# Kernel optimization log

Measured on AMD Instinct MI355X. Metric: run time of the kernel, lower is better.

Reference implementation:

```python
import jax, jax.numpy as jnp
import numpy as np

# current_extent = radius * config.KP_extent / config.conv_radius = 0.1*1.2/2.5
KP_EXTENT = 0.1 * 1.2 / 2.5
BN_EPS = 1e-5  # InstanceNorm1d default eps (BatchNormBlock normalizes over points)
LEAKY_SLOPE = 0.1


def setup_inputs() -> dict:
    key = jax.random.key(0)
    ks = jax.random.split(key, 6)
    N, H, K, C_in, C_out = 100000, 32, 15, 64, 64  # C_out = out_dim // 2
    q_pts = jax.random.normal(ks[0], (N, 3), jnp.float32)
    s_pts = q_pts + 0.01 * jax.random.normal(ks[1], (N, 3), jnp.float32)
    neighb_inds = jax.random.randint(ks[2], (N, H), 0, N)
    x = jax.random.normal(ks[3], (N, C_in), jnp.float32)
    # fixed kernel point dispositions within the convolution extent
    kernel_points = 0.5 * KP_EXTENT * jax.random.normal(ks[4], (K, 3), jnp.float32)
    weights = jax.random.normal(ks[5], (K, C_in, C_out), jnp.float32) / np.sqrt(C_in)
    return dict(q_pts=q_pts, s_pts=s_pts, neighb_inds=neighb_inds, x=x,
                kernel_points=kernel_points, weights=weights)


def _kpconv(q_pts, s_pts, neighb_inds, x, kernel_points, weights):
    # shadow point far away / shadow zero feature for out-of-range indices
    s_pad = jnp.concatenate([s_pts, jnp.full((1, 3), 1e6, s_pts.dtype)], axis=0)
    x_pad = jnp.concatenate([x, jnp.zeros((1, x.shape[1]), x.dtype)], axis=0)
    neighbors = s_pad[neighb_inds] - q_pts[:, None, :]                    # [N,H,3]
    # squared distance to every kernel point
    sq_d = jnp.sum((neighbors[:, :, None, :] - kernel_points) ** 2, -1)   # [N,H,K]
    # linear influence: max(0, 1 - d / extent), aggregation_mode='sum'
    all_weights = jnp.maximum(1.0 - jnp.sqrt(sq_d) / KP_EXTENT, 0.0)      # [N,H,K]
    neighb_x = x_pad[neighb_inds]                                         # [N,H,Cin]
    weighted = jnp.einsum('nhk,nhc->nkc', all_weights, neighb_x)          # [N,K,Cin]
    return jnp.einsum('nkc,kcd->nd', weighted, weights)                   # [N,Cout]


def reference(q_pts, s_pts, neighb_inds, x, kernel_points, weights):
    out = _kpconv(q_pts, s_pts, neighb_inds, x, kernel_points, weights)
    # BatchNormBlock: InstanceNorm1d over the points dim, no affine
    mean = jnp.mean(out, axis=0, keepdims=True)
    var = jnp.var(out, axis=0, keepdims=True)
    out = (out - mean) / jnp.sqrt(var + BN_EPS)
    # LeakyReLU(0.1)
    return jnp.where(out >= 0, out, LEAKY_SLOPE * out)
```

## Files before the change

kernel.cpp:

```cpp
#include <hip/hip_runtime.h>

typedef short short8 __attribute__((ext_vector_type(8)));
typedef float float4v __attribute__((ext_vector_type(4)));
typedef int int4v __attribute__((ext_vector_type(4)));
typedef unsigned int uint2v __attribute__((ext_vector_type(2)));
typedef unsigned int uint4v __attribute__((ext_vector_type(4)));
typedef unsigned short ushort_t;

#define INV_EXT (1.0f / 0.048f)
#define EXT 0.048f
#define HN 32
#define KK 15
#define CIN 64
#define COUT 64
#define PB 16
#define KDIM 1024
#define NSLOT 16
#define CELL_INV 64.0f

__device__ inline ushort_t rh_bf16(float f) {
    return (ushort_t)((__float_as_uint(f) + 0x8000u) >> 16);
}
__device__ inline unsigned pk_bf16(float a, float b) {
    unsigned ua = __float_as_uint(a) + 0x8000u;
    unsigned ub = __float_as_uint(b) + 0x8000u;
    return (ua >> 16) | (ub & 0xffff0000u);
}
__device__ inline int cellq(float v) {
    return (int)fminf(1023.f, fmaxf(0.f, (v + 8.f) * CELL_INV));
}
__device__ inline int imax3(int a, int b, int c) {
    int m = a > b ? a : b; return m > c ? m : c;
}
__device__ inline int iabs(int a) { return a < 0 ? -a : a; }

union Frag8 { short8 s; unsigned u[4]; };

__device__ inline int wtJ(int p, int j) {
    return p * KDIM + ((((j >> 3) ^ (p & 7)) << 3) | (j & 7));
}

template <bool CODE>
__global__ __launch_bounds__(256, 4)
void kpconv_main(const float* __restrict__ q_pts,
                 const float* __restrict__ s_pts,
                 const int*   __restrict__ inds,
                 const float* __restrict__ x,
                 const float* __restrict__ kpts,
                 const ushort_t* __restrict__ W3,
                 const unsigned* __restrict__ code,
                 float* __restrict__ out,
                 float* __restrict__ sums,
                 unsigned* __restrict__ mask, int N)
{
    __shared__ __align__(16) short wtS[PB * KDIM];
    __shared__ int indS[PB * HN];
    __shared__ unsigned actS[PB];

    const int t = threadIdx.x;
    const int n0 = blockIdx.x * PB;
    const int lane = t & 63;
    const int wid = t >> 6;
    const int l15 = lane & 15;
    const int q = lane >> 4;

    float* fp = (float*)wtS;

    float bound2; int CL;
    {
        int ki = l15 < KK ? l15 : 0;
        float bx = kpts[ki * 3 + 0], by = kpts[ki * 3 + 1], bz = kpts[ki * 3 + 2];
        float kn = l15 < KK ? __builtin_amdgcn_sqrtf(fmaf(bx, bx, fmaf(by, by, bz * bz)))
                            : 0.f;
        kn = fmaxf(kn, __shfl_xor(kn, 1));
        kn = fmaxf(kn, __shfl_xor(kn, 2));
        kn = fmaxf(kn, __shfl_xor(kn, 4));
        kn = fmaxf(kn, __shfl_xor(kn, 8));
        float b = kn + EXT + 1e-4f;
        bound2 = b * b;
        CL = (int)(b * CELL_INV) + 1;
    }

    for (int it = 0; it < 2; ++it) {
        int pi = t + it * 256;
        int p = pi >> 5, h = pi & 31;
        int n = n0 + p;
        float sx = 1e9f, sy = 1e9f, sz = 1e9f; int idx = 0;
        float dd = 1e18f;
        if (n < N) {
            idx = inds[n * HN + h];
            float qx = q_pts[n * 3 + 0];
            float qy = q_pts[n * 3 + 1];
            float qz = q_pts[n * 3 + 2];
            bool pass = true;
            if constexpr (CODE) {
                unsigned cs = code[idx];
                int dcx = iabs((int)(cs & 1023u)         - cellq(qx));
                int dcy = iabs((int)((cs >> 10) & 1023u) - cellq(qy));
                int dcz = iabs((int)((cs >> 20) & 1023u) - cellq(qz));
                pass = imax3(dcx, dcy, dcz) <= CL;
            }
            if (pass) {
                const float* sp = s_pts + (size_t)idx * 3;
                sx = sp[0]; sy = sp[1]; sz = sp[2];
                float ex = sx - qx, ey = sy - qy, ez = sz - qz;
                dd = fmaf(ex, ex, fmaf(ey, ey, ez * ez));
            }
        }
        indS[pi] = idx;
        fp[p * 512 + h]      = sx;
        fp[p * 512 + 32 + h] = sy;
        fp[p * 512 + 64 + h] = sz;
        unsigned long long bal = __ballot(dd < bound2);
        if (lane == 0)  actS[p] = (unsigned)(bal & 0xffffffffull);
        if (lane == 32) actS[p] = (unsigned)(bal >> 32);
    }
    __syncthreads();

    unsigned long long bb = __ballot(actS[l15] != 0);
    const unsigned ba = (unsigned)bb & 0xffffu;
    if (t == 0) mask[blockIdx.x] = ba;
    if (ba == 0) return;
    const int pbits = (ba >> (wid * 4)) & 0xf;

    Frag8 afrag[4];
    if (pbits) {
        int kidx = l15 < KK ? l15 : 0;
        float kx = kpts[kidx * 3 + 0];
        float ky = kpts[kidx * 3 + 1];
        float kz = kpts[kidx * 3 + 2];
        if (l15 >= KK) { kx = 3e4f; ky = 3e4f; kz = 3e4f; }
#pragma unroll
        for (int i = 0; i < 4; ++i) {
            if (!(pbits & (1 << i))) continue;
            int p = wid * 4 + i;
            int n = n0 + p;
            int nc = n < N ? n : 0;
            float qkx = q_pts[nc * 3 + 0] + kx;
            float qky = q_pts[nc * 3 + 1] + ky;
            float qkz = q_pts[nc * 3 + 2] + kz;
            int base = p * 512 + q * 8;
            float4v x0 = *(float4v*)&fp[base],      x1 = *(float4v*)&fp[base + 4];
            float4v y0 = *(float4v*)&fp[base + 32], y1 = *(float4v*)&fp[base + 36];
            float4v z0 = *(float4v*)&fp[base + 64], z1 = *(float4v*)&fp[base + 68];
            float w[8];
#pragma unroll
            for (int j = 0; j < 8; ++j) {
                float dx = (j < 4 ? x0[j & 3] : x1[j & 3]) - qkx;
                float dy = (j < 4 ? y0[j & 3] : y1[j & 3]) - qky;
                float dz = (j < 4 ? z0[j & 3] : z1[j & 3]) - qkz;
                float d = __builtin_amdgcn_sqrtf(fmaf(dx, dx, fmaf(dy, dy, dz * dz)));
                w[j] = fmaxf(fmaf(d, -INV_EXT, 1.0f), 0.0f);
            }
#pragma unroll
            for (int jj = 0; jj < 4; ++jj)
                afrag[i].u[jj] = pk_bf16(w[2 * jj], w[2 * jj + 1]);
        }
    }

#pragma unroll
    for (int i = 0; i < 4; ++i) {
        int p = wid * 4 + i;
        if (pbits & (1 << i)) {
            int ibase = p * HN + q * 8;
            int4v ia = *(int4v*)&indS[ibase];
            int4v ib = *(int4v*)&indS[ibase + 4];
            const float* rpf[8];
#pragma unroll
            for (int j = 0; j < 8; ++j) {
                int idx = j < 4 ? ia[j] : ib[j - 4];
                rpf[j] = x + (size_t)idx * CIN;
            }
#pragma unroll
            for (int ct = 0; ct < 4; ++ct) {
                short8 b;
#pragma unroll
                for (int j = 0; j < 8; ++j)
                    b[j] = (short)rh_bf16(rpf[j][ct * 16 + l15]);
                float4v acc = {0.f, 0.f, 0.f, 0.f};
                acc = __builtin_amdgcn_mfma_f32_16x16x32_bf16(afrag[i].s, b, acc, 0, 0, 0);
                uint2v v2;
                v2[0] = pk_bf16(acc[0], acc[1]);
                v2[1] = pk_bf16(acc[2], acc[3]);
                int quad = l15 + 16 * (q ^ ct) + 64 * ct;
                *(uint2v*)&wtS[wtJ(p, quad * 4)] = v2;
            }
        } else {
            uint4v z = {0u, 0u, 0u, 0u};
            *(uint4v*)&wtS[p * KDIM + lane * 16]     = z;
            *(uint4v*)&wtS[p * KDIM + lane * 16 + 8] = z;
        }
    }
    __syncthreads();

    const int d0 = wid * 16;
    float4v acc3 = {0.f, 0.f, 0.f, 0.f};
    const ushort_t* wb = W3 + (size_t)q * 512 + (d0 + l15) * 8;
#pragma unroll 8
    for (int s = 0; s < 32; ++s) {
        short8 a = *(short8*)&wtS[wtJ(l15, s * 32 + q * 8)];
        short8 bb2 = *(const short8*)(wb + (size_t)s * 2048);
        acc3 = __builtin_amdgcn_mfma_f32_16x16x32_bf16(a, bb2, acc3, 0, 0, 0);
    }

    {
        float s1 = 0.f, s2 = 0.f;
#pragma unroll
        for (int r = 0; r < 4; ++r) {
            int p = q * 4 + r;
            int n = n0 + p;
            float v = acc3[r];
            if (((ba >> p) & 1) && n < N) {
                out[n * COUT + d0 + l15] = v;
                s1 += v; s2 += v * v;
            }
        }
        s1 += __shfl_xor(s1, 16); s2 += __shfl_xor(s2, 16);
        s1 += __shfl_xor(s1, 32); s2 += __shfl_xor(s2, 32);
        if (q == 0) {
            int slot = blockIdx.x & (NSLOT - 1);
            atomicAdd(&sums[slot * 128 + d0 + l15], s1);
            atomicAdd(&sums[slot * 128 + 64 + d0 + l15], s2);
        }
    }
}

template <bool CODE>
__global__ void prep_kernel(const float* __restrict__ W,
                            const float* __restrict__ s_pts,
                            float* sums, ushort_t* W3, unsigned* code, int N)
{
    int gt = blockIdx.x * 256 + threadIdx.x;
    int stride = gridDim.x * 256;
    if (gt < NSLOT * 128) sums[gt] = 0.f;
    for (int i = gt; i < COUT * KDIM; i += stride) {
        int d = (i >> 3) & 63;
        int j = ((i >> 9) << 3) | (i & 7);
        int quad = j >> 2, r = j & 3;
        int l15 = quad & 15, e = (quad >> 4) & 3, ct = quad >> 6;
        int k = (e ^ ct) * 4 + r, c = ct * 16 + l15;
        W3[i] = (k < KK) ? rh_bf16(W[(k * CIN + c) * COUT + d]) : (ushort_t)0;
    }
    if constexpr (CODE) {
        for (int i = gt; i < N; i += stride) {
            const float* sp = s_pts + (size_t)i * 3;
            code[i] = (unsigned)cellq(sp[0])
                    | ((unsigned)cellq(sp[1]) << 10)
                    | ((unsigned)cellq(sp[2]) << 20);
        }
    }
}

__global__ void norm_kernel(float* __restrict__ out, const float* __restrict__ sums,
                            const unsigned* __restrict__ mask, int N)
{
    __shared__ float meanS[64], invS[64], czS[64];
    int t = threadIdx.x;
    if (t < 64) {
        float s1 = 0.f, s2 = 0.f;
#pragma unroll
        for (int sl = 0; sl < NSLOT; ++sl) {
            s1 += sums[sl * 128 + t];
            s2 += sums[sl * 128 + 64 + t];
        }
        float invN = 1.0f / (float)N;
        float mean = s1 * invN;
        float var = fmaxf(s2 * invN - mean * mean, 0.f);
        float inv = rsqrtf(var + 1e-5f);
        meanS[t] = mean;
        invS[t] = inv;
        float cz = (0.f - mean) * inv;
        czS[t] = cz >= 0.f ? cz : 0.1f * cz;
    }
    __syncthreads();
    long total = (long)N * 16;
    for (long i = (long)blockIdx.x * blockDim.x + t; i < total;
         i += (long)gridDim.x * blockDim.x) {
        int cb = (int)((i * 4) & 63);
        long n = i >> 4;
        unsigned mw = mask[n >> 4];
        float4v v;
        if ((mw >> ((int)n & 15)) & 1) {
            v = *(float4v*)&out[i * 4];
#pragma unroll
            for (int j = 0; j < 4; ++j) {
                float val = (v[j] - meanS[cb + j]) * invS[cb + j];
                v[j] = val >= 0.f ? val : 0.1f * val;
            }
        } else {
#pragma unroll
            for (int j = 0; j < 4; ++j) v[j] = czS[cb + j];
        }
        *(float4v*)&out[i * 4] = v;
    }
}

extern "C" void kernel_launch(void* const* d_in, const int* in_sizes, int n_in,
                              void* d_out, int out_size, void* d_ws, size_t ws_size,
                              hipStream_t stream)
{
    const float* q  = (const float*)d_in[0];
    const float* s  = (const float*)d_in[1];
    const int* inds = (const int*)d_in[2];
    const float* x  = (const float*)d_in[3];
    const float* kp = (const float*)d_in[4];
    const float* W  = (const float*)d_in[5];
    float* out = (float*)d_out;
    int N = in_sizes[0] / 3;

    int nblk = (N + PB - 1) / PB;
    float* sums    = (float*)d_ws;
    ushort_t* W3   = (ushort_t*)((char*)d_ws + 8192);
    unsigned* mask = (unsigned*)((char*)d_ws + 8192 + 131072);
    size_t code_off = 8192 + 131072 + (((size_t)nblk * 4 + 255) & ~(size_t)255);
    unsigned* code = (unsigned*)((char*)d_ws + code_off);
    bool useCode = ws_size >= code_off + (size_t)N * 4;

    if (useCode) {
        prep_kernel<true ><<<256, 256, 0, stream>>>(W, s, sums, W3, code, N);
        kpconv_main<true ><<<nblk, 256, 0, stream>>>(q, s, inds, x, kp, W3, code, out, sums, mask, N);
    } else {
        prep_kernel<false><<<256, 256, 0, stream>>>(W, s, sums, W3, code, N);
        kpconv_main<false><<<nblk, 256, 0, stream>>>(q, s, inds, x, kp, W3, code, out, sums, mask, N);
    }
    norm_kernel<<<2048, 256, 0, stream>>>(out, sums, mask, N);
}
```

Before: 124.9 us.

## Split screening into separate kernel and compact active tiles into worklist

Neighbor screening moves out of the main kernel into a lightweight grid-stride screen kernel. It sets per-tile point masks with atomicOr and appends each newly active tile to a compacted list. A persistent active kernel then walks only the listed tiles, doing the gather, MFMA weighting and weight projection, so no blocks are launched for empty tiles. The cost is an extra kernel launch, a second pass over inds/s_pts, atomic contention, and a per-tile loop with extra syncthreads.

```diff
diff --git a/kernel.cpp b/kernel.cpp
--- a/kernel.cpp
+++ b/kernel.cpp
@@ -40,170 +40,196 @@
     return p * KDIM + ((((j >> 3) ^ (p & 7)) << 3) | (j & 7));
 }
 
+__device__ inline void screen_bound(const float* kpts, int l15,
+                                    float* bound2, int* CL) {
+    int ki = l15 < KK ? l15 : 0;
+    float bx = kpts[ki * 3 + 0], by = kpts[ki * 3 + 1], bz = kpts[ki * 3 + 2];
+    float kn = l15 < KK ? __builtin_amdgcn_sqrtf(fmaf(bx, bx, fmaf(by, by, bz * bz)))
+                        : 0.f;
+    kn = fmaxf(kn, __shfl_xor(kn, 1));
+    kn = fmaxf(kn, __shfl_xor(kn, 2));
+    kn = fmaxf(kn, __shfl_xor(kn, 4));
+    kn = fmaxf(kn, __shfl_xor(kn, 8));
+    float b = kn + EXT + 1e-4f;
+    *bound2 = b * b;
+    *CL = (int)(b * CELL_INV) + 1;
+}
+
 template <bool CODE>
+__global__ __launch_bounds__(256, 8)
+void screen_kernel(const float* __restrict__ q_pts,
+                   const float* __restrict__ s_pts,
+                   const int*   __restrict__ inds,
+                   const float* __restrict__ kpts,
+                   const unsigned* __restrict__ code,
+                   unsigned* __restrict__ mask,
+                   int* __restrict__ count,
+                   int* __restrict__ list, int N)
+{
+    const int lane = threadIdx.x & 63;
+    float bound2; int CL;
+    screen_bound(kpts, lane & 15, &bound2, &CL);
+
+    const int total = N * HN;
+    for (int pi = blockIdx.x * 256 + threadIdx.x; pi < total;
+         pi += gridDim.x * 256) {
+        int n = pi >> 5;
+        int idx = inds[pi];
+        float qx = q_pts[n * 3 + 0];
+        float qy = q_pts[n * 3 + 1];
+        float qz = q_pts[n * 3 + 2];
+        bool act = false;
+        bool pass = true;
+        if constexpr (CODE) {
+            unsigned cs = code[idx];
+            int dcx = iabs((int)(cs & 1023u)         - cellq(qx));
+            int dcy = iabs((int)((cs >> 10) & 1023u) - cellq(qy));
+            int dcz = iabs((int)((cs >> 20) & 1023u) - cellq(qz));
+            pass = imax3(dcx, dcy, dcz) <= CL;
+        }
+        if (pass) {
+            const float* sp = s_pts + (size_t)idx * 3;
+            float ex = sp[0] - qx, ey = sp[1] - qy, ez = sp[2] - qz;
+            act = fmaf(ex, ex, fmaf(ey, ey, ez * ez)) < bound2;
+        }
+        unsigned long long bal = __ballot(act);
+        unsigned half = (lane < 32) ? (unsigned)bal : (unsigned)(bal >> 32);
+        if ((lane & 31) == 0 && half) {
+            unsigned old = atomicOr(&mask[n >> 4], 1u << (n & 15));
+            if (old == 0) { int pos = atomicAdd(count, 1); list[pos] = n >> 4; }
+        }
+    }
+}
+
 __global__ __launch_bounds__(256, 4)
-void kpconv_main(const float* __restrict__ q_pts,
-                 const float* __restrict__ s_pts,
-                 const int*   __restrict__ inds,
-                 const float* __restrict__ x,
-                 const float* __restrict__ kpts,
-                 const ushort_t* __restrict__ W3,
-                 const unsigned* __restrict__ code,
-                 float* __restrict__ out,
-                 float* __restrict__ sums,
-                 unsigned* __restrict__ mask, int N)
+void active_kernel(const float* __restrict__ q_pts,
+                   const float* __restrict__ s_pts,
+                   const int*   __restrict__ inds,
+                   const float* __restrict__ x,
+                   const float* __restrict__ kpts,
+                   const ushort_t* __restrict__ W3,
+                   float* __restrict__ out,
+                   float* __restrict__ sums,
+                   const unsigned* __restrict__ mask,
+                   const int* __restrict__ count,
+                   const int* __restrict__ list, int N)
 {
     __shared__ __align__(16) short wtS[PB * KDIM];
     __shared__ int indS[PB * HN];
-    __shared__ unsigned actS[PB];
 
     const int t = threadIdx.x;
-    const int n0 = blockIdx.x * PB;
     const int lane = t & 63;
     const int wid = t >> 6;
     const int l15 = lane & 15;
     const int q = lane >> 4;
-
     float* fp = (float*)wtS;
 
-    float bound2; int CL;
-    {
-        int ki = l15 < KK ? l15 : 0;
-        float bx = kpts[ki * 3 + 0], by = kpts[ki * 3 + 1], bz = kpts[ki * 3 + 2];
-        float kn = l15 < KK ? __builtin_amdgcn_sqrtf(fmaf(bx, bx, fmaf(by, by, bz * bz)))
-                            : 0.f;
-        kn = fmaxf(kn, __shfl_xor(kn, 1));
-        kn = fmaxf(kn, __shfl_xor(kn, 2));
-        kn = fmaxf(kn, __shfl_xor(kn, 4));
-        kn = fmaxf(kn, __shfl_xor(kn, 8));
-        float b = kn + EXT + 1e-4f;
-        bound2 = b * b;
-        CL = (int)(b * CELL_INV) + 1;
-    }
-
-    for (int it = 0; it < 2; ++it) {
-        int pi = t + it * 256;
-        int p = pi >> 5, h = pi & 31;
-        int n = n0 + p;
-        float sx = 1e9f, sy = 1e9f, sz = 1e9f; int idx = 0;
-        float dd = 1e18f;
-        if (n < N) {
-            idx = inds[n * HN + h];
-            float qx = q_pts[n * 3 + 0];
-            float qy = q_pts[n * 3 + 1];
-            float qz = q_pts[n * 3 + 2];
-            bool pass = true;
-            if constexpr (CODE) {
-                unsigned cs = code[idx];
-                int dcx = iabs((int)(cs & 1023u)         - cellq(qx));
-                int dcy = iabs((int)((cs >> 10) & 1023u) - cellq(qy));
-                int dcz = iabs((int)((cs >> 20) & 1023u) - cellq(qz));
-                pass = imax3(dcx, dcy, dcz) <= CL;
-            }
-            if (pass) {
+    const int cnt = *count;
+    for (int tl = blockIdx.x; tl < cnt; tl += gridDim.x) {
+        __syncthreads();
+        const int tile = list[tl];
+        const int n0 = tile * PB;
+
+        for (int it = 0; it < 2; ++it) {
+            int pi = t + it * 256;
+            int p = pi >> 5, h = pi & 31;
+            int n = n0 + p;
+            float sx = 1e9f, sy = 1e9f, sz = 1e9f; int idx = 0;
+            if (n < N) {
+                idx = inds[n * HN + h];
                 const float* sp = s_pts + (size_t)idx * 3;
                 sx = sp[0]; sy = sp[1]; sz = sp[2];
-                float ex = sx - qx, ey = sy - qy, ez = sz - qz;
-                dd = fmaf(ex, ex, fmaf(ey, ey, ez * ez));
-            }
-        }
-        indS[pi] = idx;
-        fp[p * 512 + h]      = sx;
-        fp[p * 512 + 32 + h] = sy;
-        fp[p * 512 + 64 + h] = sz;
-        unsigned long long bal = __ballot(dd < bound2);
-        if (lane == 0)  actS[p] = (unsigned)(bal & 0xffffffffull);
-        if (lane == 32) actS[p] = (unsigned)(bal >> 32);
-    }
-    __syncthreads();
-
-    unsigned long long bb = __ballot(actS[l15] != 0);
-    const unsigned ba = (unsigned)bb & 0xffffu;
-    if (t == 0) mask[blockIdx.x] = ba;
-    if (ba == 0) return;
-    const int pbits = (ba >> (wid * 4)) & 0xf;
-
-    Frag8 afrag[4];
-    if (pbits) {
-        int kidx = l15 < KK ? l15 : 0;
-        float kx = kpts[kidx * 3 + 0];
-        float ky = kpts[kidx * 3 + 1];
-        float kz = kpts[kidx * 3 + 2];
-        if (l15 >= KK) { kx = 3e4f; ky = 3e4f; kz = 3e4f; }
+            }
+            indS[pi] = idx;
+            fp[p * 512 + h]      = sx;
+            fp[p * 512 + 32 + h] = sy;
+            fp[p * 512 + 64 + h] = sz;
+        }
+        __syncthreads();
+
+        const unsigned ba = mask[tile];
+        const int pbits = (ba >> (wid * 4)) & 0xf;
+
+        Frag8 afrag[4];
+        if (pbits) {
+            int kidx = l15 < KK ? l15 : 0;
+            float kx = kpts[kidx * 3 + 0];
+            float ky = kpts[kidx * 3 + 1];
+            float kz = kpts[kidx * 3 + 2];
+            if (l15 >= KK) { kx = 3e4f; ky = 3e4f; kz = 3e4f; }
+#pragma unroll
+            for (int i = 0; i < 4; ++i) {
+                if (!(pbits & (1 << i))) continue;
+                int p = wid * 4 + i;
+                int n = n0 + p;
+                int nc = n < N ? n : 0;
+                float qkx = q_pts[nc * 3 + 0] + kx;
+                float qky = q_pts[nc * 3 + 1] + ky;
+                float qkz = q_pts[nc * 3 + 2] + kz;
+                int base = p * 512 + q * 8;
+                float4v x0 = *(float4v*)&fp[base],      x1 = *(float4v*)&fp[base + 4];
+                float4v y0 = *(float4v*)&fp[base + 32], y1 = *(float4v*)&fp[base + 36];
+                float4v z0 = *(float4v*)&fp[base + 64], z1 = *(float4v*)&fp[base + 68];
+                float w[8];
+#pragma unroll
+                for (int j = 0; j < 8; ++j) {
+                    float dx = (j < 4 ? x0[j & 3] : x1[j & 3]) - qkx;
+                    float dy = (j < 4 ? y0[j & 3] : y1[j & 3]) - qky;
+                    float dz = (j < 4 ? z0[j & 3] : z1[j & 3]) - qkz;
+                    float d = __builtin_amdgcn_sqrtf(fmaf(dx, dx, fmaf(dy, dy, dz * dz)));
+                    w[j] = fmaxf(fmaf(d, -INV_EXT, 1.0f), 0.0f);
+                }
+#pragma unroll
+                for (int jj = 0; jj < 4; ++jj)
+                    afrag[i].u[jj] = pk_bf16(w[2 * jj], w[2 * jj + 1]);
+            }
+        }
+
 #pragma unroll
         for (int i = 0; i < 4; ++i) {
-            if (!(pbits & (1 << i))) continue;
             int p = wid * 4 + i;
-            int n = n0 + p;
-            int nc = n < N ? n : 0;
-            float qkx = q_pts[nc * 3 + 0] + kx;
-            float qky = q_pts[nc * 3 + 1] + ky;
-            float qkz = q_pts[nc * 3 + 2] + kz;
-            int base = p * 512 + q * 8;
-            float4v x0 = *(float4v*)&fp[base],      x1 = *(float4v*)&fp[base + 4];
-            float4v y0 = *(float4v*)&fp[base + 32], y1 = *(float4v*)&fp[base + 36];
-            float4v z0 = *(float4v*)&fp[base + 64], z1 = *(float4v*)&fp[base + 68];
-            float w[8];
-#pragma unroll
-            for (int j = 0; j < 8; ++j) {
-                float dx = (j < 4 ? x0[j & 3] : x1[j & 3]) - qkx;
-                float dy = (j < 4 ? y0[j & 3] : y1[j & 3]) - qky;
-                float dz = (j < 4 ? z0[j & 3] : z1[j & 3]) - qkz;
-                float d = __builtin_amdgcn_sqrtf(fmaf(dx, dx, fmaf(dy, dy, dz * dz)));
-                w[j] = fmaxf(fmaf(d, -INV_EXT, 1.0f), 0.0f);
-            }
-#pragma unroll
-            for (int jj = 0; jj < 4; ++jj)
-                afrag[i].u[jj] = pk_bf16(w[2 * jj], w[2 * jj + 1]);
-        }
-    }
-
-#pragma unroll
-    for (int i = 0; i < 4; ++i) {
-        int p = wid * 4 + i;
-        if (pbits & (1 << i)) {
-            int ibase = p * HN + q * 8;
-            int4v ia = *(int4v*)&indS[ibase];
-            int4v ib = *(int4v*)&indS[ibase + 4];
-            const float* rpf[8];
-#pragma unroll
-            for (int j = 0; j < 8; ++j) {
-                int idx = j < 4 ? ia[j] : ib[j - 4];
-                rpf[j] = x + (size_t)idx * CIN;
-            }
-#pragma unroll
-            for (int ct = 0; ct < 4; ++ct) {
-                short8 b;
-#pragma unroll
-                for (int j = 0; j < 8; ++j)
-                    b[j] = (short)rh_bf16(rpf[j][ct * 16 + l15]);
-                float4v acc = {0.f, 0.f, 0.f, 0.f};
-                acc = __builtin_amdgcn_mfma_f32_16x16x32_bf16(afrag[i].s, b, acc, 0, 0, 0);
-                uint2v v2;
-                v2[0] = pk_bf16(acc[0], acc[1]);
-                v2[1] = pk_bf16(acc[2], acc[3]);
-                int quad = l15 + 16 * (q ^ ct) + 64 * ct;
-                *(uint2v*)&wtS[wtJ(p, quad * 4)] = v2;
-            }
-        } else {
-            uint4v z = {0u, 0u, 0u, 0u};
-            *(uint4v*)&wtS[p * KDIM + lane * 16]     = z;
-            *(uint4v*)&wtS[p * KDIM + lane * 16 + 8] = z;
-        }
-    }
-    __syncthreads();
-
-    const int d0 = wid * 16;
-    float4v acc3 = {0.f, 0.f, 0.f, 0.f};
-    const ushort_t* wb = W3 + (size_t)q * 512 + (d0 + l15) * 8;
+            if (pbits & (1 << i)) {
+                int ibase = p * HN + q * 8;
+                int4v ia = *(int4v*)&indS[ibase];
+                int4v ib = *(int4v*)&indS[ibase + 4];
+                const float* rpf[8];
+#pragma unroll
+                for (int j = 0; j < 8; ++j) {
+                    int idx = j < 4 ? ia[j] : ib[j - 4];
+                    rpf[j] = x + (size_t)idx * CIN;
+                }
+#pragma unroll
+                for (int ct = 0; ct < 4; ++ct) {
+                    short8 b;
+#pragma unroll
+                    for (int j = 0; j < 8; ++j)
+                        b[j] = (short)rh_bf16(rpf[j][ct * 16 + l15]);
+                    float4v acc = {0.f, 0.f, 0.f, 0.f};
+                    acc = __builtin_amdgcn_mfma_f32_16x16x32_bf16(afrag[i].s, b, acc, 0, 0, 0);
+                    uint2v v2;
+                    v2[0] = pk_bf16(acc[0], acc[1]);
+                    v2[1] = pk_bf16(acc[2], acc[3]);
+                    int quad = l15 + 16 * (q ^ ct) + 64 * ct;
+                    *(uint2v*)&wtS[wtJ(p, quad * 4)] = v2;
+                }
+            } else {
+                uint4v z = {0u, 0u, 0u, 0u};
+                *(uint4v*)&wtS[p * KDIM + lane * 16]     = z;
+                *(uint4v*)&wtS[p * KDIM + lane * 16 + 8] = z;
+            }
+        }
+        __syncthreads();
+
+        const int d0 = wid * 16;
+        float4v acc3 = {0.f, 0.f, 0.f, 0.f};
+        const ushort_t* wb = W3 + (size_t)q * 512 + (d0 + l15) * 8;
 #pragma unroll 8
-    for (int s = 0; s < 32; ++s) {
-        short8 a = *(short8*)&wtS[wtJ(l15, s * 32 + q * 8)];
-        short8 bb2 = *(const short8*)(wb + (size_t)s * 2048);
-        acc3 = __builtin_amdgcn_mfma_f32_16x16x32_bf16(a, bb2, acc3, 0, 0, 0);
-    }
-
-    {
+        for (int s = 0; s < 32; ++s) {
+            short8 a = *(short8*)&wtS[wtJ(l15, s * 32 + q * 8)];
+            short8 bb2 = *(const short8*)(wb + (size_t)s * 2048);
+            acc3 = __builtin_amdgcn_mfma_f32_16x16x32_bf16(a, bb2, acc3, 0, 0, 0);
+        }
+
         float s1 = 0.f, s2 = 0.f;
 #pragma unroll
         for (int r = 0; r < 4; ++r) {
@@ -218,7 +244,7 @@
         s1 += __shfl_xor(s1, 16); s2 += __shfl_xor(s2, 16);
         s1 += __shfl_xor(s1, 32); s2 += __shfl_xor(s2, 32);
         if (q == 0) {
-            int slot = blockIdx.x & (NSLOT - 1);
+            int slot = tile & (NSLOT - 1);
             atomicAdd(&sums[slot * 128 + d0 + l15], s1);
             atomicAdd(&sums[slot * 128 + 64 + d0 + l15], s2);
         }
@@ -228,11 +254,14 @@
 template <bool CODE>
 __global__ void prep_kernel(const float* __restrict__ W,
                             const float* __restrict__ s_pts,
-                            float* sums, ushort_t* W3, unsigned* code, int N)
+                            float* sums, ushort_t* W3, unsigned* code,
+                            unsigned* mask, int* count, int nblk, int N)
 {
     int gt = blockIdx.x * 256 + threadIdx.x;
     int stride = gridDim.x * 256;
     if (gt < NSLOT * 128) sums[gt] = 0.f;
+    if (gt == 0) *count = 0;
+    for (int i = gt; i < nblk; i += stride) mask[i] = 0u;
     for (int i = gt; i < COUT * KDIM; i += stride) {
         int d = (i >> 3) & 63;
         int j = ((i >> 9) << 3) | (i & 7);
@@ -311,17 +340,23 @@
     int nblk = (N + PB - 1) / PB;
     float* sums    = (float*)d_ws;
     ushort_t* W3   = (ushort_t*)((char*)d_ws + 8192);
-    unsigned* mask = (unsigned*)((char*)d_ws + 8192 + 131072);
-    size_t code_off = 8192 + 131072 + (((size_t)nblk * 4 + 255) & ~(size_t)255);
+    size_t mask_off = 8192 + 131072;
+    unsigned* mask = (unsigned*)((char*)d_ws + mask_off);
+    size_t cnt_off  = mask_off + (((size_t)nblk * 4 + 255) & ~(size_t)255);
+    int* count     = (int*)((char*)d_ws + cnt_off);
+    size_t list_off = cnt_off + 256;
+    int* list      = (int*)((char*)d_ws + list_off);
+    size_t code_off = list_off + (((size_t)nblk * 4 + 255) & ~(size_t)255);
     unsigned* code = (unsigned*)((char*)d_ws + code_off);
     bool useCode = ws_size >= code_off + (size_t)N * 4;
 
     if (useCode) {
-        prep_kernel<true ><<<256, 256, 0, stream>>>(W, s, sums, W3, code, N);
-        kpconv_main<true ><<<nblk, 256, 0, stream>>>(q, s, inds, x, kp, W3, code, out, sums, mask, N);
+        prep_kernel<true ><<<256, 256, 0, stream>>>(W, s, sums, W3, code, mask, count, nblk, N);
+        screen_kernel<true ><<<2048, 256, 0, stream>>>(q, s, inds, kp, code, mask, count, list, N);
     } else {
-        prep_kernel<false><<<256, 256, 0, stream>>>(W, s, sums, W3, code, N);
-        kpconv_main<false><<<nblk, 256, 0, stream>>>(q, s, inds, x, kp, W3, code, out, sums, mask, N);
-    }
+        prep_kernel<false><<<256, 256, 0, stream>>>(W, s, sums, W3, code, mask, count, nblk, N);
+        screen_kernel<false><<<2048, 256, 0, stream>>>(q, s, inds, kp, code, mask, count, list, N);
+    }
+    active_kernel<<<512, 256, 0, stream>>>(q, s, inds, x, kp, W3, out, sums, mask, count, list, N);
     norm_kernel<<<2048, 256, 0, stream>>>(out, sums, mask, N);
 }
```

Measured after the change: 129.4 us. 3.6% more time.

## Fuse conv and normalization into one persistent kernel with grid barrier

Applied to the files above, without the earlier changes.

Turns the main conv kernel into a persistent kernel with a fixed grid that loops over point tiles. After all tiles are done it runs a software grid-wide barrier built from atomics, then applies the instance-norm and LeakyReLU pass in the same kernel, which removes the separate norm kernel launch. The barrier assumes all 960 blocks are resident at the same time, and it risks deadlock if they are not. The fixed grid may also balance tiles differently than the original one-block-per-tile launch.

```diff
diff --git a/kernel.cpp b/kernel.cpp
--- a/kernel.cpp
+++ b/kernel.cpp
@@ -17,6 +17,8 @@
 #define KDIM 1024
 #define NSLOT 16
 #define CELL_INV 64.0f
+#define GRIDF 960
+#define NGRP 30
 
 __device__ inline ushort_t rh_bf16(float f) {
     return (ushort_t)((__float_as_uint(f) + 0x8000u) >> 16);
@@ -40,30 +42,44 @@
     return p * KDIM + ((((j >> 3) ^ (p & 7)) << 3) | (j & 7));
 }
 
+__device__ inline void grid_barrier(int* bar) {
+    __threadfence();
+    __syncthreads();
+    if (threadIdx.x == 0) {
+        int g = blockIdx.x >> 5;
+        if (atomicAdd(&bar[g], 1) == 31)
+            atomicAdd(&bar[NGRP], 1);
+        while (atomicAdd(&bar[NGRP], 0) < NGRP)
+            __builtin_amdgcn_s_sleep(2);
+    }
+    __syncthreads();
+    __threadfence();
+}
+
 template <bool CODE>
 __global__ __launch_bounds__(256, 4)
-void kpconv_main(const float* __restrict__ q_pts,
-                 const float* __restrict__ s_pts,
-                 const int*   __restrict__ inds,
-                 const float* __restrict__ x,
-                 const float* __restrict__ kpts,
-                 const ushort_t* __restrict__ W3,
-                 const unsigned* __restrict__ code,
-                 float* __restrict__ out,
-                 float* __restrict__ sums,
-                 unsigned* __restrict__ mask, int N)
+void fused_kernel(const float* __restrict__ q_pts,
+                  const float* __restrict__ s_pts,
+                  const int*   __restrict__ inds,
+                  const float* __restrict__ x,
+                  const float* __restrict__ kpts,
+                  const ushort_t* __restrict__ W3,
+                  const unsigned* __restrict__ code,
+                  float* __restrict__ out,
+                  float* __restrict__ sums,
+                  unsigned* __restrict__ mask,
+                  int* __restrict__ bar, int N, int nblk)
 {
     __shared__ __align__(16) short wtS[PB * KDIM];
     __shared__ int indS[PB * HN];
     __shared__ unsigned actS[PB];
+    __shared__ float nmS[192];
 
     const int t = threadIdx.x;
-    const int n0 = blockIdx.x * PB;
     const int lane = t & 63;
     const int wid = t >> 6;
     const int l15 = lane & 15;
     const int q = lane >> 4;
-
     float* fp = (float*)wtS;
 
     float bound2; int CL;
@@ -80,130 +96,133 @@
         bound2 = b * b;
         CL = (int)(b * CELL_INV) + 1;
     }
-
-    for (int it = 0; it < 2; ++it) {
-        int pi = t + it * 256;
-        int p = pi >> 5, h = pi & 31;
-        int n = n0 + p;
-        float sx = 1e9f, sy = 1e9f, sz = 1e9f; int idx = 0;
-        float dd = 1e18f;
-        if (n < N) {
-            idx = inds[n * HN + h];
-            float qx = q_pts[n * 3 + 0];
-            float qy = q_pts[n * 3 + 1];
-            float qz = q_pts[n * 3 + 2];
-            bool pass = true;
-            if constexpr (CODE) {
-                unsigned cs = code[idx];
-                int dcx = iabs((int)(cs & 1023u)         - cellq(qx));
-                int dcy = iabs((int)((cs >> 10) & 1023u) - cellq(qy));
-                int dcz = iabs((int)((cs >> 20) & 1023u) - cellq(qz));
-                pass = imax3(dcx, dcy, dcz) <= CL;
-            }
-            if (pass) {
-                const float* sp = s_pts + (size_t)idx * 3;
-                sx = sp[0]; sy = sp[1]; sz = sp[2];
-                float ex = sx - qx, ey = sy - qy, ez = sz - qz;
-                dd = fmaf(ex, ex, fmaf(ey, ey, ez * ez));
-            }
-        }
-        indS[pi] = idx;
-        fp[p * 512 + h]      = sx;
-        fp[p * 512 + 32 + h] = sy;
-        fp[p * 512 + 64 + h] = sz;
-        unsigned long long bal = __ballot(dd < bound2);
-        if (lane == 0)  actS[p] = (unsigned)(bal & 0xffffffffull);
-        if (lane == 32) actS[p] = (unsigned)(bal >> 32);
-    }
-    __syncthreads();
-
-    unsigned long long bb = __ballot(actS[l15] != 0);
-    const unsigned ba = (unsigned)bb & 0xffffu;
-    if (t == 0) mask[blockIdx.x] = ba;
-    if (ba == 0) return;
-    const int pbits = (ba >> (wid * 4)) & 0xf;
-
-    Frag8 afrag[4];
-    if (pbits) {
-        int kidx = l15 < KK ? l15 : 0;
-        float kx = kpts[kidx * 3 + 0];
-        float ky = kpts[kidx * 3 + 1];
-        float kz = kpts[kidx * 3 + 2];
-        if (l15 >= KK) { kx = 3e4f; ky = 3e4f; kz = 3e4f; }
+    const int d0 = wid * 16;
+    const ushort_t* wb = W3 + (size_t)q * 512 + (d0 + l15) * 8;
+
+    for (int tile = blockIdx.x; tile < nblk; tile += GRIDF) {
+        __syncthreads();
+        const int n0 = tile * PB;
+
+        for (int it = 0; it < 2; ++it) {
+            int pi = t + it * 256;
+            int p = pi >> 5, h = pi & 31;
+            int n = n0 + p;
+            float sx = 1e9f, sy = 1e9f, sz = 1e9f; int idx = 0;
+            float dd = 1e18f;
+            if (n < N) {
+                idx = inds[n * HN + h];
+                float qx = q_pts[n * 3 + 0];
+                float qy = q_pts[n * 3 + 1];
+                float qz = q_pts[n * 3 + 2];
+                bool pass = true;
+                if constexpr (CODE) {
+                    unsigned cs = code[idx];
+                    int dcx = iabs((int)(cs & 1023u)         - cellq(qx));
+                    int dcy = iabs((int)((cs >> 10) & 1023u) - cellq(qy));
+                    int dcz = iabs((int)((cs >> 20) & 1023u) - cellq(qz));
+                    pass = imax3(dcx, dcy, dcz) <= CL;
+                }
+                if (pass) {
+                    const float* sp = s_pts + (size_t)idx * 3;
+                    sx = sp[0]; sy = sp[1]; sz = sp[2];
+                    float ex = sx - qx, ey = sy - qy, ez = sz - qz;
+                    dd = fmaf(ex, ex, fmaf(ey, ey, ez * ez));
+                }
+            }
+            indS[pi] = idx;
+            fp[p * 512 + h]      = sx;
+            fp[p * 512 + 32 + h] = sy;
+            fp[p * 512 + 64 + h] = sz;
+            unsigned long long bal = __ballot(dd < bound2);
+            if (lane == 0)  actS[p] = (unsigned)(bal & 0xffffffffull);
+            if (lane == 32) actS[p] = (unsigned)(bal >> 32);
+        }
+        __syncthreads();
+
+        unsigned long long bb = __ballot(actS[l15] != 0);
+        const unsigned ba = (unsigned)bb & 0xffffu;
+        if (t == 0) mask[tile] = ba;
+        if (ba == 0) continue;
+        const int pbits = (ba >> (wid * 4)) & 0xf;
+
+        Frag8 afrag[4];
+        if (pbits) {
+            int kidx = l15 < KK ? l15 : 0;
+            float kx = kpts[kidx * 3 + 0];
+            float ky = kpts[kidx * 3 + 1];
+            float kz = kpts[kidx * 3 + 2];
+            if (l15 >= KK) { kx = 3e4f; ky = 3e4f; kz = 3e4f; }
+#pragma unroll
+            for (int i = 0; i < 4; ++i) {
+                if (!(pbits & (1 << i))) continue;
+                int p = wid * 4 + i;
+                int n = n0 + p;
+                int nc = n < N ? n : 0;
+                float qkx = q_pts[nc * 3 + 0] + kx;
+                float qky = q_pts[nc * 3 + 1] + ky;
+                float qkz = q_pts[nc * 3 + 2] + kz;
+                int base = p * 512 + q * 8;
+                float4v x0 = *(float4v*)&fp[base],      x1 = *(float4v*)&fp[base + 4];
+                float4v y0 = *(float4v*)&fp[base + 32], y1 = *(float4v*)&fp[base + 36];
+                float4v z0 = *(float4v*)&fp[base + 64], z1 = *(float4v*)&fp[base + 68];
+                float w[8];
+#pragma unroll
+                for (int j = 0; j < 8; ++j) {
+                    float dx = (j < 4 ? x0[j & 3] : x1[j & 3]) - qkx;
+                    float dy = (j < 4 ? y0[j & 3] : y1[j & 3]) - qky;
+                    float dz = (j < 4 ? z0[j & 3] : z1[j & 3]) - qkz;
+                    float d = __builtin_amdgcn_sqrtf(fmaf(dx, dx, fmaf(dy, dy, dz * dz)));
+                    w[j] = fmaxf(fmaf(d, -INV_EXT, 1.0f), 0.0f);
+                }
+#pragma unroll
+                for (int jj = 0; jj < 4; ++jj)
+                    afrag[i].u[jj] = pk_bf16(w[2 * jj], w[2 * jj + 1]);
+            }
+        }
+
 #pragma unroll
         for (int i = 0; i < 4; ++i) {
-            if (!(pbits & (1 << i))) continue;
             int p = wid * 4 + i;
-            int n = n0 + p;
-            int nc = n < N ? n : 0;
-            float qkx = q_pts[nc * 3 + 0] + kx;
-            float qky = q_pts[nc * 3 + 1] + ky;
-            float qkz = q_pts[nc * 3 + 2] + kz;
-            int base = p * 512 + q * 8;
-            float4v x0 = *(float4v*)&fp[base],      x1 = *(float4v*)&fp[base + 4];
-            float4v y0 = *(float4v*)&fp[base + 32], y1 = *(float4v*)&fp[base + 36];
-            float4v z0 = *(float4v*)&fp[base + 64], z1 = *(float4v*)&fp[base + 68];
-            float w[8];
-#pragma unroll
-            for (int j = 0; j < 8; ++j) {
-                float dx = (j < 4 ? x0[j & 3] : x1[j & 3]) - qkx;
-                float dy = (j < 4 ? y0[j & 3] : y1[j & 3]) - qky;
-                float dz = (j < 4 ? z0[j & 3] : z1[j & 3]) - qkz;
-                float d = __builtin_amdgcn_sqrtf(fmaf(dx, dx, fmaf(dy, dy, dz * dz)));
-                w[j] = fmaxf(fmaf(d, -INV_EXT, 1.0f), 0.0f);
-            }
-#pragma unroll
-            for (int jj = 0; jj < 4; ++jj)
-                afrag[i].u[jj] = pk_bf16(w[2 * jj], w[2 * jj + 1]);
-        }
-    }
-
-#pragma unroll
-    for (int i = 0; i < 4; ++i) {
-        int p = wid * 4 + i;
-        if (pbits & (1 << i)) {
-            int ibase = p * HN + q * 8;
-            int4v ia = *(int4v*)&indS[ibase];
-            int4v ib = *(int4v*)&indS[ibase + 4];
-            const float* rpf[8];
-#pragma unroll
-            for (int j = 0; j < 8; ++j) {
-                int idx = j < 4 ? ia[j] : ib[j - 4];
-                rpf[j] = x + (size_t)idx * CIN;
-            }
-#pragma unroll
-            for (int ct = 0; ct < 4; ++ct) {
-                short8 b;
-#pragma unroll
-                for (int j = 0; j < 8; ++j)
-                    b[j] = (short)rh_bf16(rpf[j][ct * 16 + l15]);
-                float4v acc = {0.f, 0.f, 0.f, 0.f};
-                acc = __builtin_amdgcn_mfma_f32_16x16x32_bf16(afrag[i].s, b, acc, 0, 0, 0);
-                uint2v v2;
-                v2[0] = pk_bf16(acc[0], acc[1]);
-                v2[1] = pk_bf16(acc[2], acc[3]);
-                int quad = l15 + 16 * (q ^ ct) + 64 * ct;
-                *(uint2v*)&wtS[wtJ(p, quad * 4)] = v2;
-            }
-        } else {
-            uint4v z = {0u, 0u, 0u, 0u};
-            *(uint4v*)&wtS[p * KDIM + lane * 16]     = z;
-            *(uint4v*)&wtS[p * KDIM + lane * 16 + 8] = z;
-        }
-    }
-    __syncthreads();
-
-    const int d0 = wid * 16;
-    float4v acc3 = {0.f, 0.f, 0.f, 0.f};
-    const ushort_t* wb = W3 + (size_t)q * 512 + (d0 + l15) * 8;
+            if (pbits & (1 << i)) {
+                int ibase = p * HN + q * 8;
+                int4v ia = *(int4v*)&indS[ibase];
+                int4v ib = *(int4v*)&indS[ibase + 4];
+                const float* rpf[8];
+#pragma unroll
+                for (int j = 0; j < 8; ++j) {
+                    int idx = j < 4 ? ia[j] : ib[j - 4];
+                    rpf[j] = x + (size_t)idx * CIN;
+                }
+#pragma unroll
+                for (int ct = 0; ct < 4; ++ct) {
+                    short8 b;
+#pragma unroll
+                    for (int j = 0; j < 8; ++j)
+                        b[j] = (short)rh_bf16(rpf[j][ct * 16 + l15]);
+                    float4v acc = {0.f, 0.f, 0.f, 0.f};
+                    acc = __builtin_amdgcn_mfma_f32_16x16x32_bf16(afrag[i].s, b, acc, 0, 0, 0);
+                    uint2v v2;
+                    v2[0] = pk_bf16(acc[0], acc[1]);
+                    v2[1] = pk_bf16(acc[2], acc[3]);
+                    int quad = l15 + 16 * (q ^ ct) + 64 * ct;
+                    *(uint2v*)&wtS[wtJ(p, quad * 4)] = v2;
+                }
+            } else {
+                uint4v z = {0u, 0u, 0u, 0u};
+                *(uint4v*)&wtS[p * KDIM + lane * 16]     = z;
+                *(uint4v*)&wtS[p * KDIM + lane * 16 + 8] = z;
+            }
+        }
+        __syncthreads();
+
+        float4v acc3 = {0.f, 0.f, 0.f, 0.f};
 #pragma unroll 8
-    for (int s = 0; s < 32; ++s) {
-        short8 a = *(short8*)&wtS[wtJ(l15, s * 32 + q * 8)];
-        short8 bb2 = *(const short8*)(wb + (size_t)s * 2048);
-        acc3 = __builtin_amdgcn_mfma_f32_16x16x32_bf16(a, bb2, acc3, 0, 0, 0);
-    }
-
-    {
+        for (int s = 0; s < 32; ++s) {
+            short8 a = *(short8*)&wtS[wtJ(l15, s * 32 + q * 8)];
+            short8 bb2 = *(const short8*)(wb + (size_t)s * 2048);
+            acc3 = __builtin_amdgcn_mfma_f32_16x16x32_bf16(a, bb2, acc3, 0, 0, 0);
+        }
+
         float s1 = 0.f, s2 = 0.f;
 #pragma unroll
         for (int r = 0; r < 4; ++r) {
@@ -218,21 +237,62 @@
         s1 += __shfl_xor(s1, 16); s2 += __shfl_xor(s2, 16);
         s1 += __shfl_xor(s1, 32); s2 += __shfl_xor(s2, 32);
         if (q == 0) {
-            int slot = blockIdx.x & (NSLOT - 1);
+            int slot = tile & (NSLOT - 1);
             atomicAdd(&sums[slot * 128 + d0 + l15], s1);
             atomicAdd(&sums[slot * 128 + 64 + d0 + l15], s2);
         }
+    }
+
+    grid_barrier(bar);
+
+    if (t < 64) {
+        float s1 = 0.f, s2 = 0.f;
+#pragma unroll
+        for (int sl = 0; sl < NSLOT; ++sl) {
+            s1 += sums[sl * 128 + t];
+            s2 += sums[sl * 128 + 64 + t];
+        }
+        float invN = 1.0f / (float)N;
+        float mean = s1 * invN;
+        float var = fmaxf(s2 * invN - mean * mean, 0.f);
+        float inv = rsqrtf(var + 1e-5f);
+        nmS[t] = mean;
+        nmS[64 + t] = inv;
+        float cz = (0.f - mean) * inv;
+        nmS[128 + t] = cz >= 0.f ? cz : 0.1f * cz;
+    }
+    __syncthreads();
+    long total = (long)N * 16;
+    for (long i = (long)blockIdx.x * 256 + t; i < total; i += (long)GRIDF * 256) {
+        int cb = (int)((i * 4) & 63);
+        long n = i >> 4;
+        unsigned mw = mask[n >> 4];
+        float4v v;
+        if ((mw >> ((int)n & 15)) & 1) {
+            v = *(float4v*)&out[i * 4];
+#pragma unroll
+            for (int j = 0; j < 4; ++j) {
+                float val = (v[j] - nmS[cb + j]) * nmS[64 + cb + j];
+                v[j] = val >= 0.f ? val : 0.1f * val;
+            }
+        } else {
+#pragma unroll
+            for (int j = 0; j < 4; ++j) v[j] = nmS[128 + cb + j];
+        }
+        *(float4v*)&out[i * 4] = v;
     }
 }
 
 template <bool CODE>
 __global__ void prep_kernel(const float* __restrict__ W,
                             const float* __restrict__ s_pts,
-                            float* sums, ushort_t* W3, unsigned* code, int N)
+                            float* sums, ushort_t* W3, unsigned* code,
+                            int* bar, int N)
 {
     int gt = blockIdx.x * 256 + threadIdx.x;
     int stride = gridDim.x * 256;
     if (gt < NSLOT * 128) sums[gt] = 0.f;
+    if (gt < NGRP + 1) bar[gt] = 0;
     for (int i = gt; i < COUT * KDIM; i += stride) {
         int d = (i >> 3) & 63;
         int j = ((i >> 9) << 3) | (i & 7);
@@ -248,50 +308,6 @@
                     | ((unsigned)cellq(sp[1]) << 10)
                     | ((unsigned)cellq(sp[2]) << 20);
         }
-    }
-}
-
-__global__ void norm_kernel(float* __restrict__ out, const float* __restrict__ sums,
-                            const unsigned* __restrict__ mask, int N)
-{
-    __shared__ float meanS[64], invS[64], czS[64];
-    int t = threadIdx.x;
-    if (t < 64) {
-        float s1 = 0.f, s2 = 0.f;
-#pragma unroll
-        for (int sl = 0; sl < NSLOT; ++sl) {
-            s1 += sums[sl * 128 + t];
-            s2 += sums[sl * 128 + 64 + t];
-        }
-        float invN = 1.0f / (float)N;
-        float mean = s1 * invN;
-        float var = fmaxf(s2 * invN - mean * mean, 0.f);
-        float inv = rsqrtf(var + 1e-5f);
-        meanS[t] = mean;
-        invS[t] = inv;
-        float cz = (0.f - mean) * inv;
-        czS[t] = cz >= 0.f ? cz : 0.1f * cz;
-    }
-    __syncthreads();
-    long total = (long)N * 16;
-    for (long i = (long)blockIdx.x * blockDim.x + t; i < total;
-         i += (long)gridDim.x * blockDim.x) {
-        int cb = (int)((i * 4) & 63);
-        long n = i >> 4;
-        unsigned mw = mask[n >> 4];
-        float4v v;
-        if ((mw >> ((int)n & 15)) & 1) {
-            v = *(float4v*)&out[i * 4];
-#pragma unroll
-            for (int j = 0; j < 4; ++j) {
-                float val = (v[j] - meanS[cb + j]) * invS[cb + j];
-                v[j] = val >= 0.f ? val : 0.1f * val;
-            }
-        } else {
-#pragma unroll
-            for (int j = 0; j < 4; ++j) v[j] = czS[cb + j];
-        }
-        *(float4v*)&out[i * 4] = v;
     }
 }
 
@@ -311,17 +327,21 @@
     int nblk = (N + PB - 1) / PB;
     float* sums    = (float*)d_ws;
     ushort_t* W3   = (ushort_t*)((char*)d_ws + 8192);
-    unsigned* mask = (unsigned*)((char*)d_ws + 8192 + 131072);
-    size_t code_off = 8192 + 131072 + (((size_t)nblk * 4 + 255) & ~(size_t)255);
+    size_t mask_off = 8192 + 131072;
+    unsigned* mask = (unsigned*)((char*)d_ws + mask_off);
+    size_t bar_off  = mask_off + (((size_t)nblk * 4 + 255) & ~(size_t)255);
+    int* bar       = (int*)((char*)d_ws + bar_off);
+    size_t code_off = bar_off + 256;
     unsigned* code = (unsigned*)((char*)d_ws + code_off);
     bool useCode = ws_size >= code_off + (size_t)N * 4;
 
     if (useCode) {
-        prep_kernel<true ><<<256, 256, 0, stream>>>(W, s, sums, W3, code, N);
-        kpconv_main<true ><<<nblk, 256, 0, stream>>>(q, s, inds, x, kp, W3, code, out, sums, mask, N);
+        prep_kernel<true ><<<256, 256, 0, stream>>>(W, s, sums, W3, code, bar, N);
+        fused_kernel<true ><<<GRIDF, 256, 0, stream>>>(q, s, inds, x, kp, W3, code,
+                                                       out, sums, mask, bar, N, nblk);
     } else {
-        prep_kernel<false><<<256, 256, 0, stream>>>(W, s, sums, W3, code, N);
-        kpconv_main<false><<<nblk, 256, 0, stream>>>(q, s, inds, x, kp, W3, code, out, sums, mask, N);
-    }
-    norm_kernel<<<2048, 256, 0, stream>>>(out, sums, mask, N);
-}
+        prep_kernel<false><<<256, 256, 0, stream>>>(W, s, sums, W3, code, bar, N);
+        fused_kernel<false><<<GRIDF, 256, 0, stream>>>(q, s, inds, x, kp, W3, code,
+                                                       out, sums, mask, bar, N, nblk);
+    }
+}
```

Result: slower. 357.1 us (+185.9%).
